# Kernel tuning notes

Hardware: AMD Instinct MI355X
Metric: run time of the kernel (lower is better)

Reference implementation:

```python
import jax, jax.numpy as jnp
import numpy as np

B, L = 512, 8192          # batch, document length
N = 128                   # output_sentence_num
S = 256                   # output_sentence_len
DELIM = 5                 # delimiter token
PAD = 0                   # pad_word
CUT_HEAD = False
VOCAB = 100


def setup_inputs() -> dict:
    key = jax.random.key(0)
    x = jax.random.randint(key, (B, L), 0, VOCAB, dtype=jnp.int32)
    return {"x": x}


def reference(x):
    b, l = x.shape
    # right-padded row: original tokens + one trailing delimiter, shape [B, L+1]
    rpad = jnp.concatenate([x, jnp.full((b, 1), DELIM, x.dtype)], axis=1)
    # segment id of rpad position j = number of delimiters in x[:j]
    cum = jnp.cumsum((x == DELIM).astype(jnp.int32), axis=1)           # [B, L]
    seg = jnp.concatenate([jnp.zeros((b, 1), jnp.int32), cum], axis=1)  # [B, L+1]
    seg = jnp.minimum(seg, N - 1)  # segments >= N-1 merged into last chunk (tail merge)
    j = jnp.arange(l + 1, dtype=jnp.int32)
    bidx = jnp.arange(b)[:, None]
    # start index of each segment (min j with seg==k); unused segments stay at L+1
    starts = jnp.full((b, N), l + 1, jnp.int32)
    starts = starts.at[bidx, seg].min(jnp.broadcast_to(j, (b, l + 1)))
    pos = j[None, :] - jnp.take_along_axis(starts, seg, axis=1)  # offset within chunk
    # chunk sizes (number of rpad positions per segment)
    sizes = jnp.zeros((b, N), jnp.int32).at[bidx, seg].add(jnp.ones((b, l + 1), jnp.int32))
    size_here = jnp.take_along_axis(sizes, seg, axis=1)
    # size-1 chunks (lone delimiter == empty sentence) are filled with pad_word
    vals = jnp.where(size_here == 1, jnp.int32(PAD), rpad)
    if CUT_HEAD:
        p = pos - 1
        valid = (pos >= 1) & (pos <= S - 1)  # chunk[1:S], then padded to S
    else:
        p = pos
        valid = pos <= S - 1                 # chunk[:S]
    # scatter into [B, N, S]; invalid positions routed out-of-bounds and dropped
    k_idx = jnp.where(valid, seg, N)
    p_idx = jnp.where(valid, p, S)
    otp = jnp.full((b, N, S), PAD, x.dtype)
    otp = otp.at[bidx, k_idx, p_idx].set(vals, mode='drop')
    # lengths / mask (tf.count_nonzero semantics; pad_word == 0)
    len_sent = jnp.sum((otp != 0).astype(jnp.int32), axis=2)   # [B, N]
    len_doc = jnp.sum((len_sent != 0).astype(jnp.int32), axis=1)  # [B]
    mask = (jnp.arange(S)[None, None, :] < len_sent[..., None]).astype(jnp.float32)
    return otp, len_doc, mask
```

## Files before the change

kernel.cpp:

```cpp
#include <hip/hip_runtime.h>

#define B_ 512
#define L_ 8192
#define N_ 128
#define S_ 256
#define DELIM_ 5
#define T_ 512
#define NW_ (T_ / 64)
#define PER_ (L_ / T_)

__global__ __launch_bounds__(T_) void split_kernel(const int* __restrict__ x,
                                                   float* __restrict__ otp,
                                                   float* __restrict__ len_doc,
                                                   float* __restrict__ mask) {
    const int b = blockIdx.x;
    const int t = threadIdx.x;
    const int lane = t & 63;
    const int w = t >> 6;
    const int* __restrict__ row = x + (size_t)b * L_;

    __shared__ int s_wsum[NW_];
    __shared__ int s_dpos[N_ - 1];
    __shared__ int s_start[N_];
    __shared__ int s_cl[N_];
    __shared__ int s_doc[NW_];

    const int base = t * PER_;
    int c = 0;
#pragma unroll
    for (int i = 0; i < PER_; ++i) c += (row[base + i] == DELIM_);

    int v = c;
#pragma unroll
    for (int d = 1; d < 64; d <<= 1) {
        int n = __shfl_up(v, d, 64);
        if (lane >= d) v += n;
    }
    if (lane == 63) s_wsum[w] = v;
    __syncthreads();

    int woff = 0, m = 0;
#pragma unroll
    for (int i = 0; i < NW_; ++i) {
        const int sv = s_wsum[i];
        if (i < w) woff += sv;
        m += sv;
    }
    const int off = woff + v - c;

    if (c > 0 && off < N_ - 1) {
        int o = off;
        for (int i = 0; i < PER_; ++i) {
            if (row[base + i] == DELIM_) {
                if (o < N_ - 1) s_dpos[o] = base + i;
                ++o;
            }
        }
    }
    __syncthreads();

    if (t < N_) {
        const int k = t;
        const int mc = (m < N_ - 1) ? m : (N_ - 1);
        int start = 0, cl = 0;
        if (k <= mc) {
            start = (k == 0) ? 0 : (s_dpos[k - 1] + 1);
            const int end = (k < mc) ? s_dpos[k] : L_;
            const int size = end - start + 1;
            cl = (size <= 1) ? 0 : (size < S_ ? size : S_);
        }
        s_start[k] = start;
        s_cl[k] = cl;
    }
    __syncthreads();

    float* __restrict__ otp_b = otp + (size_t)b * N_ * S_;
    float* __restrict__ msk_b = mask + (size_t)b * N_ * S_;
    int doccnt = 0;
    for (int i = 0; i < (N_ / NW_); ++i) {
        const int k = i * NW_ + w;
        const int start = s_start[k];
        const int cl = s_cl[k];
        const int s0 = lane * 4;
        float tf[4];
        int nz = 0;
#pragma unroll
        for (int j = 0; j < 4; ++j) {
            const int e = s0 + j;
            int tok = 0;
            if (e < cl) {
                const int g = start + e;
                tok = (g < L_) ? row[g] : DELIM_;
            }
            tf[j] = (float)tok;
            nz += (tok != 0);
        }
        int len = nz;
#pragma unroll
        for (int d = 32; d >= 1; d >>= 1) len += __shfl_xor(len, d, 64);

        *(float4*)(otp_b + (size_t)k * S_ + s0) =
            make_float4(tf[0], tf[1], tf[2], tf[3]);
        *(float4*)(msk_b + (size_t)k * S_ + s0) =
            make_float4(s0 < len ? 1.0f : 0.0f, s0 + 1 < len ? 1.0f : 0.0f,
                        s0 + 2 < len ? 1.0f : 0.0f, s0 + 3 < len ? 1.0f : 0.0f);
        doccnt += (len > 0);
    }

    if (lane == 0) s_doc[w] = doccnt;
    __syncthreads();
    if (t == 0) {
        int d = 0;
#pragma unroll
        for (int i = 0; i < NW_; ++i) d += s_doc[i];
        len_doc[b] = (float)d;
    }
}

extern "C" void kernel_launch(void* const* d_in, const int* in_sizes, int n_in,
                              void* d_out, int out_size, void* d_ws, size_t ws_size,
                              hipStream_t stream) {
    const int* x = (const int*)d_in[0];
    float* out = (float*)d_out;

    float* otp = out;
    float* len_doc = out + (size_t)B_ * N_ * S_;
    float* mask = len_doc + B_;

    split_kernel<<<B_, T_, 0, stream>>>(x, otp, len_doc, mask);
}
```

Before: 143.3 us.

## Use 1024 threads with int4 coalesced loads and packed dual-counter scan

Doubles the block size to 1024 threads. Each thread now loads two coalesced int4 vectors instead of a strided 16-element run, and the two delimiter counts are packed into one 32-bit scan to find both offsets at once. Delimiter positions are written from registers without reloading the row. The per-sentence nonzero count uses ballot+popcount instead of a shuffle reduction, and the output loop is unrolled. The cost is higher register pressure at 1024 threads, and the packed 16-bit fields limit the range of each count.

After: 142.5 us. Within noise of the previous version (-0.6%).

```diff
diff --git a/kernel.cpp b/kernel.cpp
--- a/kernel.cpp
+++ b/kernel.cpp
@@ -5,9 +5,8 @@
 #define N_ 128
 #define S_ 256
 #define DELIM_ 5
-#define T_ 512
+#define T_ 1024
 #define NW_ (T_ / 64)
-#define PER_ (L_ / T_)
 
 __global__ __launch_bounds__(T_) void split_kernel(const int* __restrict__ x,
                                                    float* __restrict__ otp,
@@ -25,12 +24,13 @@
     __shared__ int s_cl[N_];
     __shared__ int s_doc[NW_];
 
-    const int base = t * PER_;
-    int c = 0;
-#pragma unroll
-    for (int i = 0; i < PER_; ++i) c += (row[base + i] == DELIM_);
+    const int4 r0 = ((const int4*)row)[t];
+    const int4 r1 = ((const int4*)row)[t + T_];
+    const int c0 = (r0.x == DELIM_) + (r0.y == DELIM_) + (r0.z == DELIM_) + (r0.w == DELIM_);
+    const int c1 = (r1.x == DELIM_) + (r1.y == DELIM_) + (r1.z == DELIM_) + (r1.w == DELIM_);
+    const int packed = c0 | (c1 << 16);
 
-    int v = c;
+    int v = packed;
 #pragma unroll
     for (int d = 1; d < 64; d <<= 1) {
         int n = __shfl_up(v, d, 64);
@@ -39,23 +39,34 @@
     if (lane == 63) s_wsum[w] = v;
     __syncthreads();
 
-    int woff = 0, m = 0;
+    int woff = 0, tot = 0;
 #pragma unroll
     for (int i = 0; i < NW_; ++i) {
         const int sv = s_wsum[i];
         if (i < w) woff += sv;
-        m += sv;
+        tot += sv;
     }
-    const int off = woff + v - c;
+    const int pre = woff + v - packed;
+    const int c0tot = tot & 0xffff;
+    const int m = c0tot + (tot >> 16);
+    const int off0 = pre & 0xffff;
+    const int off1 = c0tot + (pre >> 16);
 
-    if (c > 0 && off < N_ - 1) {
-        int o = off;
-        for (int i = 0; i < PER_; ++i) {
-            if (row[base + i] == DELIM_) {
-                if (o < N_ - 1) s_dpos[o] = base + i;
-                ++o;
-            }
-        }
+    if (c0 > 0 && off0 < N_ - 1) {
+        int o = off0;
+        const int p = 4 * t;
+        if (r0.x == DELIM_) { if (o < N_ - 1) s_dpos[o] = p;     ++o; }
+        if (r0.y == DELIM_) { if (o < N_ - 1) s_dpos[o] = p + 1; ++o; }
+        if (r0.z == DELIM_) { if (o < N_ - 1) s_dpos[o] = p + 2; ++o; }
+        if (r0.w == DELIM_) { if (o < N_ - 1) s_dpos[o] = p + 3; ++o; }
+    }
+    if (c1 > 0 && off1 < N_ - 1) {
+        int o = off1;
+        const int p = 4 * T_ + 4 * t;
+        if (r1.x == DELIM_) { if (o < N_ - 1) s_dpos[o] = p;     ++o; }
+        if (r1.y == DELIM_) { if (o < N_ - 1) s_dpos[o] = p + 1; ++o; }
+        if (r1.z == DELIM_) { if (o < N_ - 1) s_dpos[o] = p + 2; ++o; }
+        if (r1.w == DELIM_) { if (o < N_ - 1) s_dpos[o] = p + 3; ++o; }
     }
     __syncthreads();
 
@@ -77,13 +88,14 @@
     float* __restrict__ otp_b = otp + (size_t)b * N_ * S_;
     float* __restrict__ msk_b = mask + (size_t)b * N_ * S_;
     int doccnt = 0;
+#pragma unroll
     for (int i = 0; i < (N_ / NW_); ++i) {
         const int k = i * NW_ + w;
         const int start = s_start[k];
         const int cl = s_cl[k];
         const int s0 = lane * 4;
         float tf[4];
-        int nz = 0;
+        int len = 0;
 #pragma unroll
         for (int j = 0; j < 4; ++j) {
             const int e = s0 + j;
@@ -93,11 +105,8 @@
                 tok = (g < L_) ? row[g] : DELIM_;
             }
             tf[j] = (float)tok;
-            nz += (tok != 0);
+            len += __popcll(__ballot(tok != 0));
         }
-        int len = nz;
-#pragma unroll
-        for (int d = 32; d >= 1; d >>= 1) len += __shfl_xor(len, d, 64);
 
         *(float4*)(otp_b + (size_t)k * S_ + s0) =
             make_float4(tf[0], tf[1], tf[2], tf[3]);
```
